# Kernel tuning notes

Hardware: AMD Instinct MI355X
Metric: run time of the kernel (lower is better)

Reference implementation:

```python
import jax, jax.numpy as jnp
import numpy as np

PATCH_SIZES = (16, 32, 48, 64)
RES_IDX = (0, 1, 2, 3)  # min(int(s*4/3), 3) for s in 0..3
QUANT_RESI = 0.5
BETA = 0.25
D = 32      # embedding_dim == input channels
V = 2048    # vocab_size
G = 8       # GroupNorm groups
EPS = 1e-5


def conv3(x, w, b):
    y = jax.lax.conv_general_dilated(x, w, (1, 1), 'SAME', dimension_numbers=('NCHW', 'OIHW', 'NCHW'))
    return y + b[None, :, None, None]


def group_norm(x, gamma, beta):
    n, c, h, w = x.shape
    xr = x.reshape(n, G, c // G, h, w)
    mu = xr.mean(axis=(2, 3, 4), keepdims=True)
    var = xr.var(axis=(2, 3, 4), keepdims=True)
    xn = ((xr - mu) * jax.lax.rsqrt(var + EPS)).reshape(n, c, h, w)
    return xn * gamma[None, :, None, None] + beta[None, :, None, None]


def conv_block(x, w1, b1, gamma, beta, w2, b2):
    h = conv3(x, w1, b1)
    h = jax.nn.gelu(group_norm(h, gamma, beta), approximate=False)
    return conv3(h, w2, b2)


def _forward(x, emb, pw1, pb1, pg, pbt, pw2, pb2, rw1, rb1, rg, rbt, rw2, rb2):
    B, C, H, W = x.shape
    acc = jnp.zeros_like(x)
    total_loss = jnp.zeros((), x.dtype)
    idx_list = []
    for s, p in enumerate(PATCH_SIZES):
        nh, nw = H // p, W // p
        # unfold: non-overlapping patches -> (B*N, C, p, p), N row-major over (nh, nw)
        patches = (x - acc).reshape(B, C, nh, p, nw, p).transpose(0, 2, 4, 1, 3, 5).reshape(B * nh * nw, C, p, p)
        z = conv_block(patches, pw1[s], pb1[s], pg[s], pbt[s], pw2[s], pb2[s])
        zf = z.reshape(-1, D)  # raw row-major reshape, exactly as the torch code does
        d = (zf * zf).sum(1, keepdims=True) + (emb * emb).sum(1) - 2.0 * (zf @ emb.T)
        idx = jnp.argmin(d, axis=1)
        zq = emb[idx].reshape(z.shape)
        loss = jnp.mean((jax.lax.stop_gradient(zq) - z) ** 2) + BETA * jnp.mean((zq - jax.lax.stop_gradient(z)) ** 2)
        total_loss = total_loss + loss
        zq = z + jax.lax.stop_gradient(zq - z)  # straight-through estimator
        r = RES_IDX[s]
        zq = zq * (1.0 - QUANT_RESI) + conv_block(zq, rw1[r], rb1[r], rg[r], rbt[r], rw2[r], rb2[r]) * QUANT_RESI
        # fold: exact inverse of unfold (patch sizes divide H, W)
        decoded = zq.reshape(B, nh, nw, C, p, p).transpose(0, 3, 1, 4, 2, 5).reshape(B, C, H, W)
        acc = acc + decoded
        idx_list.append(idx.reshape(B, -1))
    return (jax.nn.sigmoid(acc), *idx_list, total_loss)


def setup_inputs() -> dict:
    key = jax.random.key(0)
    ks = jax.random.split(key, 4)
    S = len(PATCH_SIZES)
    x = jax.random.normal(ks[0], (1, D, 384, 384), dtype=jnp.float32)
    emb = jax.random.uniform(ks[1], (V, D), jnp.float32, -1.0 / V, 1.0 / V)

    def wset(k):
        k1, k2, k3, k4 = jax.random.split(k, 4)
        return (jax.random.normal(k1, (S, D, D, 3, 3), jnp.float32) * 0.05,
                jax.random.normal(k2, (S, D), jnp.float32) * 0.02,
                jnp.ones((S, D), jnp.float32),
                jnp.zeros((S, D), jnp.float32),
                jax.random.normal(k3, (S, D, D, 3, 3), jnp.float32) * 0.05,
                jax.random.normal(k4, (S, D), jnp.float32) * 0.02)

    pw1, pb1, pg, pbt, pw2, pb2 = wset(ks[2])
    rw1, rb1, rg, rbt, rw2, rb2 = wset(ks[3])
    return {"x": x, "emb": emb,
            "pw1": pw1, "pb1": pb1, "pg": pg, "pbt": pbt, "pw2": pw2, "pb2": pb2,
            "rw1": rw1, "rb1": rb1, "rg": rg, "rbt": rbt, "rw2": rw2, "rb2": rb2}


def reference(x, emb, pw1, pb1, pg, pbt, pw2, pb2, rw1, rb1, rg, rbt, rw2, rb2):
    return _forward(x, emb, pw1, pb1, pg, pbt, pw2, pb2, rw1, rb1, rg, rbt, rw2, rb2)
```

## Files before the change

### kernel.cpp

```cpp
#include <hip/hip_runtime.h>
#include <cmath>

#define WIDTH 384
#define HW 147456
#define CHW 4718592
#define NCH 32
#define NV 2048
#define NROWS 147456

typedef short vshort8 __attribute__((ext_vector_type(8)));
typedef float vfloat4 __attribute__((ext_vector_type(4)));

__device__ inline unsigned short bf_split(float x, float& back) {
  unsigned int b; __builtin_memcpy(&b, &x, 4);
  unsigned int r = (b + 0x7FFFu + ((b >> 16) & 1u)) >> 16;
  unsigned int bb = r << 16; float f; __builtin_memcpy(&f, &bb, 4);
  back = f; return (unsigned short)r;
}

template <int SQ>
__device__ float np_pw(const float* a, int n, float mu) {
  if (n < 8) {
    float res = 0.0f;
    for (int i = 0; i < n; i++) {
      float v = a[i];
      if (SQ) { float d = __fsub_rn(v, mu); v = __fmul_rn(d, d); }
      res = __fadd_rn(res, v);
    }
    return res;
  }
  if (n <= 128) {
    float r[8];
#pragma unroll
    for (int j = 0; j < 8; j++) {
      float v = a[j];
      if (SQ) { float d = __fsub_rn(v, mu); v = __fmul_rn(d, d); }
      r[j] = v;
    }
    int i;
    for (i = 8; i + 8 <= n; i += 8) {
#pragma unroll
      for (int j = 0; j < 8; j++) {
        float v = a[i + j];
        if (SQ) { float d = __fsub_rn(v, mu); v = __fmul_rn(d, d); }
        r[j] = __fadd_rn(r[j], v);
      }
    }
    float res = __fadd_rn(__fadd_rn(__fadd_rn(r[0], r[1]), __fadd_rn(r[2], r[3])),
                          __fadd_rn(__fadd_rn(r[4], r[5]), __fadd_rn(r[6], r[7])));
    for (; i < n; i++) {
      float v = a[i];
      if (SQ) { float d = __fsub_rn(v, mu); v = __fmul_rn(d, d); }
      res = __fadd_rn(res, v);
    }
    return res;
  }
  int n2 = n / 2; n2 -= n2 % 8;
  return __fadd_rn(np_pw<SQ>(a, n2, mu), np_pw<SQ>(a + n2, n - n2, mu));
}

__global__ __launch_bounds__(256) void prep_kernel(
    const float* __restrict__ pw1, const float* __restrict__ pw2,
    const float* __restrict__ rw1, const float* __restrict__ rw2,
    const float* __restrict__ emb, float* __restrict__ wt, float* __restrict__ ee,
    unsigned short* __restrict__ eh, unsigned short* __restrict__ el) {
  int t = blockIdx.x * 256 + threadIdx.x;
  if (t < 147456) {
    int layer = t / 9216, r = t % 9216;
    int k = r / 32, co = r % 32;
    int set = layer >> 2, s = layer & 3;
    const float* src = set == 0 ? pw1 : set == 1 ? pw2 : set == 2 ? rw1 : rw2;
    wt[t] = src[s * 9216 + co * 288 + k];
  } else if (t < 147456 + NV) {
    int v = t - 147456;
    const float* e = emb + v * 32;
    float r[8];
#pragma unroll
    for (int j = 0; j < 8; j++) r[j] = __fmul_rn(e[j], e[j]);
#pragma unroll
    for (int i = 8; i < 32; i += 8)
#pragma unroll
      for (int j = 0; j < 8; j++) r[j] = __fadd_rn(r[j], __fmul_rn(e[i + j], e[i + j]));
    ee[v] = __fadd_rn(__fadd_rn(__fadd_rn(r[0], r[1]), __fadd_rn(r[2], r[3])),
                      __fadd_rn(__fadd_rn(r[4], r[5]), __fadd_rn(r[6], r[7])));
  } else if (t < 147456 + NV + 65536) {
    int idx = t - 147456 - NV;
    float x = emb[idx], hb;
    eh[idx] = bf_split(x, hb);
    float lb;
    el[idx] = bf_split(__fsub_rn(x, hb), lb);
  }
}

template <int MODE>
__global__ __launch_bounds__(192, 3) void conv32_kernel(
    const float* __restrict__ in, const float* __restrict__ x,
    const float* __restrict__ accin, float* __restrict__ outb,
    const float* __restrict__ zqb, float* __restrict__ acc,
    const float* __restrict__ wt, const float* __restrict__ bias, int p, int nw) {
  int t = blockIdx.x * 192 + threadIdx.x;
  int pp = p * p;
  int px = t % p; int t1 = t / p;
  int py = t1 % p;
  int n  = t1 / p;
  int i = n / nw, j = n % nw;

  int off[9]; bool msk[9];
#pragma unroll
  for (int dy = 0; dy < 3; dy++) {
    int ly = py + dy - 1;
    bool vy = (unsigned)ly < (unsigned)p;
    int cy = vy ? ly : 0;
#pragma unroll
    for (int dx = 0; dx < 3; dx++) {
      int lx = px + dx - 1;
      bool vx = (unsigned)lx < (unsigned)p;
      int cx = vx ? lx : 0;
      msk[dy * 3 + dx] = vy && vx;
      if (MODE == 1) off[dy * 3 + dx] = (i * p + cy) * WIDTH + (j * p + cx);
      else           off[dy * 3 + dx] = cy * p + cx;
    }
  }

  const float* pin = (MODE == 1) ? nullptr : in + (size_t)n * NCH * pp;

  float a[NCH];
#pragma unroll
  for (int co = 0; co < NCH; co++) a[co] = 0.0f;

  float tv[9], tn[9];
#pragma unroll
  for (int k = 0; k < 9; k++) {
    float v;
    if (MODE == 1) {
      size_t ad = (size_t)off[k];
      v = __fsub_rn(x[ad], accin[ad]);
    } else {
      v = pin[off[k]];
    }
    tv[k] = msk[k] ? v : 0.0f;
  }

  for (int ci = 0; ci < NCH; ci++) {
    if (ci + 1 < NCH) {
#pragma unroll
      for (int k = 0; k < 9; k++) {
        float v;
        if (MODE == 1) {
          size_t ad = (size_t)(ci + 1) * HW + off[k];
          v = __fsub_rn(x[ad], accin[ad]);
        } else {
          v = pin[(size_t)(ci + 1) * pp + off[k]];
        }
        tn[k] = msk[k] ? v : 0.0f;
      }
    }
    const float* wp = wt + ci * 288;
#pragma unroll
    for (int k = 0; k < 9; k++) {
#pragma unroll
      for (int co = 0; co < NCH; co++)
        a[co] = fmaf(tv[k], wp[k * 32 + co], a[co]);
    }
#pragma unroll
    for (int k = 0; k < 9; k++) tv[k] = tn[k];
  }

#pragma unroll
  for (int co = 0; co < NCH; co++) {
    float r = __fadd_rn(a[co], bias[co]);
    if (MODE == 2) {
      size_t img = (size_t)co * HW + (size_t)(i * p + py) * WIDTH + (j * p + px);
      size_t pt  = (size_t)n * NCH * pp + (size_t)co * pp + (size_t)py * p + px;
      float dec = __fadd_rn(__fmul_rn(zqb[pt], 0.5f), __fmul_rn(r, 0.5f));
      acc[img] = __fadd_rn(acc[img], dec);
    } else {
      outb[(size_t)n * NCH * pp + (size_t)co * pp + (size_t)py * p + px] = r;
    }
  }
}

__global__ __launch_bounds__(64) void gn_stats_kernel(
    const float* __restrict__ buf, float2* __restrict__ stats,
    int p, int C, int chunk) {
  int tid = threadIdx.x;
  int gpw = 64 / C;
  int gi = tid / C, cl = tid % C;
  int grp = blockIdx.x * gpw + gi;
  int pp = p * p, ne = 4 * pp;
  const float* base = buf + ((size_t)(grp >> 3) * NCH + (size_t)(grp & 7) * 4) * pp
                      + (size_t)cl * chunk;

  float s = np_pw<0>(base, chunk, 0.0f);
  for (int m = 1; m < C; m <<= 1) s = __fadd_rn(s, __shfl_xor(s, m, 64));
  float mu = __fdiv_rn(s, (float)ne);

  float s2 = np_pw<1>(base, chunk, mu);
  for (int m = 1; m < C; m <<= 1) s2 = __fadd_rn(s2, __shfl_xor(s2, m, 64));

  if (cl == 0) {
    float var = __fdiv_rn(s2, (float)ne);
    float rs = __fdiv_rn(1.0f, __fsqrt_rn(__fadd_rn(var, 1e-5f)));
    stats[grp] = make_float2(mu, rs);
  }
}

__global__ __launch_bounds__(256) void gn_gelu_kernel(
    float* __restrict__ buf, const float2* __restrict__ stats,
    const float* __restrict__ gamma, const float* __restrict__ beta, int p) {
  int t = blockIdx.x * 256 + threadIdx.x;
  int pp = p * p;
  int t2 = t / pp;
  int c = t2 % NCH;
  int n = t2 / NCH;
  float2 st = stats[n * 8 + (c >> 2)];
  float v = __fadd_rn(__fmul_rn(__fmul_rn(__fsub_rn(buf[t], st.x), st.y), gamma[c]), beta[c]);
  float tt = __fdiv_rn(v, 1.41421356237309504880f);
  float e = (float)erf((double)tt);
  buf[t] = __fmul_rn(__fmul_rn(0.5f, v), __fadd_rn(1.0f, e));
}

__global__ __launch_bounds__(192) void zsplit_kernel(
    const float* __restrict__ z, unsigned short* __restrict__ zh,
    unsigned short* __restrict__ zl, float* __restrict__ zz) {
  int r = blockIdx.x * 192 + threadIdx.x;
  const float* zr = z + (size_t)r * 32;
  float zv[32];
#pragma unroll
  for (int q = 0; q < 32; q++) zv[q] = zr[q];

  float rr[8];
#pragma unroll
  for (int j = 0; j < 8; j++) rr[j] = __fmul_rn(zv[j], zv[j]);
#pragma unroll
  for (int i = 8; i < 32; i += 8)
#pragma unroll
    for (int j = 0; j < 8; j++) rr[j] = __fadd_rn(rr[j], __fmul_rn(zv[i + j], zv[i + j]));
  zz[r] = __fadd_rn(__fadd_rn(__fadd_rn(rr[0], rr[1]), __fadd_rn(rr[2], rr[3])),
                    __fadd_rn(__fadd_rn(rr[4], rr[5]), __fadd_rn(rr[6], rr[7])));

  unsigned short hbits[32], lbits[32];
#pragma unroll
  for (int q = 0; q < 32; q++) {
    float hb;
    hbits[q] = bf_split(zv[q], hb);
    float lb;
    lbits[q] = bf_split(__fsub_rn(zv[q], hb), lb);
  }
#pragma unroll
  for (int c = 0; c < 4; c++) {
    vshort8 hv, lv;
#pragma unroll
    for (int j = 0; j < 8; j++) { hv[j] = (short)hbits[c * 8 + j]; lv[j] = (short)lbits[c * 8 + j]; }
    *(vshort8*)(zh + (size_t)r * 32 + c * 8) = hv;
    *(vshort8*)(zl + (size_t)r * 32 + c * 8) = lv;
  }
}

__global__ __launch_bounds__(576, 5) void gemm_min_kernel(
    const unsigned short* __restrict__ ZH, const unsigned short* __restrict__ ZL,
    const float* __restrict__ ZZ,
    const unsigned short* __restrict__ EH, const unsigned short* __restrict__ EL,
    const float* __restrict__ EE,
    float* __restrict__ BD, float* __restrict__ B2, int* __restrict__ I1) {
  __shared__ float ee_l[2048];
  int tid = threadIdx.x;
  for (int i = tid; i < 2048; i += 576) ee_l[i] = EE[i];
  __syncthreads();

  int wid = tid / 64, lane = tid & 63;
  int t0 = blockIdx.x * 18 + wid * 2;
  int lr = lane & 15, lg = lane >> 4;

  vshort8 azh0 = *(const vshort8*)(ZH + (size_t)(t0 * 16 + lr) * 32 + 8 * lg);
  vshort8 azl0 = *(const vshort8*)(ZL + (size_t)(t0 * 16 + lr) * 32 + 8 * lg);
  vshort8 azh1 = *(const vshort8*)(ZH + (size_t)((t0 + 1) * 16 + lr) * 32 + 8 * lg);
  vshort8 azl1 = *(const vshort8*)(ZL + (size_t)((t0 + 1) * 16 + lr) * 32 + 8 * lg);
  float zzv[8];
#pragma unroll
  for (int r = 0; r < 4; r++) {
    zzv[r]     = ZZ[t0 * 16 + 4 * lg + r];
    zzv[4 + r] = ZZ[(t0 + 1) * 16 + 4 * lg + r];
  }

  float b1[8], b2[8]; int i1[8];
#pragma unroll
  for (int r = 0; r < 8; r++) { b1[r] = 3.402823466e+38f; b2[r] = 3.402823466e+38f; i1[r] = 0; }

  vshort8 nbeh = *(const vshort8*)(EH + (size_t)lr * 32 + 8 * lg);
  vshort8 nbel = *(const vshort8*)(EL + (size_t)lr * 32 + 8 * lg);

  for (int ct = 0; ct < 128; ct++) {
    vshort8 beh = nbeh, bel = nbel;
    if (ct + 1 < 128) {
      nbeh = *(const vshort8*)(EH + (size_t)((ct + 1) * 16 + lr) * 32 + 8 * lg);
      nbel = *(const vshort8*)(EL + (size_t)((ct + 1) * 16 + lr) * 32 + 8 * lg);
    }
    vfloat4 acc0 = {0.0f, 0.0f, 0.0f, 0.0f};
    acc0 = __builtin_amdgcn_mfma_f32_16x16x32_bf16(azh0, beh, acc0, 0, 0, 0);
    acc0 = __builtin_amdgcn_mfma_f32_16x16x32_bf16(azh0, bel, acc0, 0, 0, 0);
    acc0 = __builtin_amdgcn_mfma_f32_16x16x32_bf16(azl0, beh, acc0, 0, 0, 0);
    vfloat4 acc1 = {0.0f, 0.0f, 0.0f, 0.0f};
    acc1 = __builtin_amdgcn_mfma_f32_16x16x32_bf16(azh1, beh, acc1, 0, 0, 0);
    acc1 = __builtin_amdgcn_mfma_f32_16x16x32_bf16(azh1, bel, acc1, 0, 0, 0);
    acc1 = __builtin_amdgcn_mfma_f32_16x16x32_bf16(azl1, beh, acc1, 0, 0, 0);
    int col = ct * 16 + lr;
    float eev = ee_l[col];
#pragma unroll
    for (int r = 0; r < 4; r++) {
      float d = (zzv[r] + eev) - 2.0f * acc0[r];
      if (d < b1[r]) { b2[r] = b1[r]; b1[r] = d; i1[r] = col; }
      else b2[r] = fminf(b2[r], d);
      float d1 = (zzv[4 + r] + eev) - 2.0f * acc1[r];
      if (d1 < b1[4 + r]) { b2[4 + r] = b1[4 + r]; b1[4 + r] = d1; i1[4 + r] = col; }
      else b2[4 + r] = fminf(b2[4 + r], d1);
    }
  }

  for (int m = 1; m < 16; m <<= 1) {
#pragma unroll
    for (int r = 0; r < 8; r++) {
      float ob1 = __shfl_xor(b1[r], m, 64);
      int   oi1 = __shfl_xor(i1[r], m, 64);
      float ob2 = __shfl_xor(b2[r], m, 64);
      bool aw = (b1[r] < ob1) || (b1[r] == ob1 && i1[r] < oi1);
      float lo = aw ? ob1 : b1[r];
      b1[r] = aw ? b1[r] : ob1;
      i1[r] = aw ? i1[r] : oi1;
      b2[r] = fminf(fminf(b2[r], ob2), lo);
    }
  }

  if (lr == 0) {
#pragma unroll
    for (int r = 0; r < 4; r++) {
      int row0 = t0 * 16 + 4 * lg + r;
      BD[row0] = b1[r]; B2[row0] = b2[r]; I1[row0] = i1[r];
      int row1 = (t0 + 1) * 16 + 4 * lg + r;
      BD[row1] = b1[4 + r]; B2[row1] = b2[4 + r]; I1[row1] = i1[4 + r];
    }
  }
}

__global__ __launch_bounds__(192) void finalize_kernel(
    const float* __restrict__ z, const float* __restrict__ emb,
    const float* __restrict__ EE, const float* __restrict__ ZZ,
    const float* __restrict__ BD, const float* __restrict__ B2,
    const int* __restrict__ I1, float* __restrict__ zq,
    float* __restrict__ idxout, double* __restrict__ part) {
  __shared__ double red[192];
  int tid = threadIdx.x;
  int lane = tid & 63;
  int r = blockIdx.x * 192 + tid;
  const float* zr = z + (size_t)r * 32;

  float zv[32];
#pragma unroll
  for (int q = 0; q < 32; q++) zv[q] = zr[q];

  float bd = BD[r];
  int bi = I1[r];
  float margin = __fadd_rn(1.0e-6f, __fmul_rn(5.0e-7f, fabsf(bd)));
  bool flagged = (B2[r] - bd) <= margin;

  unsigned long long mask = __ballot(flagged);
  while (mask) {
    int l = __ffsll((long long)mask) - 1;
    mask &= mask - 1;
    float zb[32];
#pragma unroll
    for (int q = 0; q < 32; q++) zb[q] = __shfl(zv[q], l, 64);
    int rl = __shfl(r, l, 64);
    float zzb = ZZ[rl];
    float bestd = 3.402823466e+38f;
    int bestv = NV;
    for (int k = 0; k < 32; k++) {
      int v = lane + 64 * k;
      const float* e0 = emb + (size_t)v * 32;
      float m = 0.0f;
#pragma unroll
      for (int q = 0; q < 32; q++) m = fmaf(zb[q], e0[q], m);
      float d = __fsub_rn(__fadd_rn(zzb, EE[v]), __fmul_rn(2.0f, m));
      if (d < bestd) { bestd = d; bestv = v; }
    }
    for (int mm = 1; mm < 64; mm <<= 1) {
      float od = __shfl_xor(bestd, mm, 64);
      int ov = __shfl_xor(bestv, mm, 64);
      if (od < bestd || (od == bestd && ov < bestv)) { bestd = od; bestv = ov; }
    }
    if (lane == l) bi = bestv;
  }

  double sse = 0.0;
  const float* ep = emb + (size_t)bi * 32;
#pragma unroll
  for (int q = 0; q < 32; q++) {
    float e = ep[q];
    zq[(size_t)r * 32 + q] = e;
    double dd = (double)e - (double)zv[q];
    sse += dd * dd;
  }
  idxout[r] = (float)bi;

  red[tid] = sse;
  __syncthreads();
  if (tid < 64) red[tid] = red[tid] + red[tid + 64] + red[tid + 128];
  __syncthreads();
  for (int st = 32; st > 0; st >>= 1) {
    if (tid < st) red[tid] += red[tid + st];
    __syncthreads();
  }
  if (tid == 0) part[blockIdx.x] = red[0];
}

__global__ __launch_bounds__(256) void sigmoid_kernel(
    const float* __restrict__ acc, float* __restrict__ out) {
  int t = blockIdx.x * 256 + threadIdx.x;
  out[t] = (float)(1.0 / (1.0 + exp(-(double)acc[t])));
}

__global__ void loss_kernel(const double* __restrict__ part, float* __restrict__ out) {
  double tot = 0.0;
  for (int s = 0; s < 4; s++) {
    double sse = 0.0;
    for (int b = 0; b < 768; b++) sse += part[s * 1024 + b];
    tot += 1.25 * sse / 4718592.0;
  }
  out[0] = (float)tot;
}

extern "C" void kernel_launch(void* const* d_in, const int* in_sizes, int n_in,
                              void* d_out, int out_size, void* d_ws, size_t ws_size,
                              hipStream_t stream) {
  const float* X   = (const float*)d_in[0];
  const float* EMB = (const float*)d_in[1];
  const float* PW1 = (const float*)d_in[2];
  const float* PB1 = (const float*)d_in[3];
  const float* PG  = (const float*)d_in[4];
  const float* PBT = (const float*)d_in[5];
  const float* PW2 = (const float*)d_in[6];
  const float* PB2 = (const float*)d_in[7];
  const float* RW1 = (const float*)d_in[8];
  const float* RB1 = (const float*)d_in[9];
  const float* RG  = (const float*)d_in[10];
  const float* RBT = (const float*)d_in[11];
  const float* RW2 = (const float*)d_in[12];
  const float* RB2 = (const float*)d_in[13];
  float* out = (float*)d_out;

  char* w = (char*)d_ws;
  float*          EE    = (float*)(w);
  float*          WT    = (float*)(w + 8192UL);
  unsigned short* EH    = (unsigned short*)(w + 598016UL);
  unsigned short* EL    = (unsigned short*)(w + 729088UL);
  float2*         STATS = (float2*)(w + 860160UL);
  double*         PART  = (double*)(w + 897024UL);
  float*          ZZ    = (float*)(w + 929792UL);
  float*          BD    = (float*)(w + 1519616UL);
  float*          B2    = (float*)(w + 2109440UL);
  int*            I1    = (int*)(w + 2699264UL);
  unsigned short* ZH    = (unsigned short*)(w + 3289088UL);
  unsigned short* ZL    = (unsigned short*)(w + 12726272UL);
  float*          P     = (float*)(w + 22163456UL);
  float*          H     = (float*)(w + 41037824UL);
  float*          ACC   = (float*)(w + 59912192UL);

  hipMemsetAsync(ACC, 0, 18874368UL, stream);
  prep_kernel<<<840, 256, 0, stream>>>(PW1, PW2, RW1, RW2, EMB, WT, EE, EH, EL);

  const int PS[4] = {16, 32, 48, 64};
  for (int s = 0; s < 4; s++) {
    int p = PS[s], nw = 384 / p, N = nw * nw;
    int C = (p == 16) ? 8 : (p == 32) ? 32 : 64;
    int chunk = (4 * p * p) / C;
    int gblocks = (N * 8 * C) / 64;
    const float* wt_p1 = WT + (0 * 4 + s) * 9216;
    const float* wt_p2 = WT + (1 * 4 + s) * 9216;
    const float* wt_r1 = WT + (2 * 4 + s) * 9216;
    const float* wt_r2 = WT + (3 * 4 + s) * 9216;

    conv32_kernel<1><<<768, 192, 0, stream>>>(nullptr, X, ACC, H, nullptr, nullptr,
                                              wt_p1, PB1 + s * 32, p, nw);
    gn_stats_kernel<<<gblocks, 64, 0, stream>>>(H, STATS, p, C, chunk);
    gn_gelu_kernel<<<18432, 256, 0, stream>>>(H, STATS, PG + s * 32, PBT + s * 32, p);
    conv32_kernel<0><<<768, 192, 0, stream>>>(H, nullptr, nullptr, P, nullptr, nullptr,
                                              wt_p2, PB2 + s * 32, p, nw);
    zsplit_kernel<<<768, 192, 0, stream>>>(P, ZH, ZL, ZZ);
    gemm_min_kernel<<<512, 576, 0, stream>>>(ZH, ZL, ZZ, EH, EL, EE, BD, B2, I1);
    finalize_kernel<<<768, 192, 0, stream>>>(P, EMB, EE, ZZ, BD, B2, I1, H,
                                             out + 4718592 + s * 147456, PART + s * 1024);
    conv32_kernel<0><<<768, 192, 0, stream>>>(H, nullptr, nullptr, P, nullptr, nullptr,
                                              wt_r1, RB1 + s * 32, p, nw);
    gn_stats_kernel<<<gblocks, 64, 0, stream>>>(P, STATS, p, C, chunk);
    gn_gelu_kernel<<<18432, 256, 0, stream>>>(P, STATS, RG + s * 32, RBT + s * 32, p);
    conv32_kernel<2><<<768, 192, 0, stream>>>(P, nullptr, nullptr, nullptr, H, ACC,
                                              wt_r2, RB2 + s * 32, p, nw);
  }

  sigmoid_kernel<<<18432, 256, 0, stream>>>(ACC, out);
  loss_kernel<<<1, 1, 0, stream>>>(PART, out + 5308416);
}
```

Baseline: 2.205 ms.

## Fuse VQ finalize step into the GEMM argmin kernel

Merges finalize_kernel into gemm_min_kernel: best/second-best distances and indices stay in shared memory instead of going through global BD/B2/I1 buffers. Near-tie rows get an exact fp32 recheck by one wave per row, which now reads z from global and EE from shared memory. Then the block writes zq and idx and reduces the SSE partials. This removes a kernel launch and the global round trip, but adds shared memory use and serialized per-wave recheck work inside the GEMM kernel, which may lower occupancy.

```diff
diff --git a/kernel.cpp b/kernel.cpp
--- a/kernel.cpp
+++ b/kernel.cpp
@@ -261,9 +261,13 @@
     const unsigned short* __restrict__ ZH, const unsigned short* __restrict__ ZL,
     const float* __restrict__ ZZ,
     const unsigned short* __restrict__ EH, const unsigned short* __restrict__ EL,
-    const float* __restrict__ EE,
-    float* __restrict__ BD, float* __restrict__ B2, int* __restrict__ I1) {
+    const float* __restrict__ EE, const float* __restrict__ z,
+    const float* __restrict__ emb, float* __restrict__ zq,
+    float* __restrict__ idxout, double* __restrict__ part) {
   __shared__ float ee_l[2048];
+  __shared__ int bi_l[288];
+  __shared__ int fl_l[288];
+  __shared__ double red[576];
   int tid = threadIdx.x;
   for (int i = tid; i < 2048; i += 576) ee_l[i] = EE[i];
   __syncthreads();
@@ -334,53 +338,36 @@
   if (lr == 0) {
 #pragma unroll
     for (int r = 0; r < 4; r++) {
-      int row0 = t0 * 16 + 4 * lg + r;
-      BD[row0] = b1[r]; B2[row0] = b2[r]; I1[row0] = i1[r];
-      int row1 = (t0 + 1) * 16 + 4 * lg + r;
-      BD[row1] = b1[4 + r]; B2[row1] = b2[4 + r]; I1[row1] = i1[4 + r];
-    }
-  }
-}
-
-__global__ __launch_bounds__(192) void finalize_kernel(
-    const float* __restrict__ z, const float* __restrict__ emb,
-    const float* __restrict__ EE, const float* __restrict__ ZZ,
-    const float* __restrict__ BD, const float* __restrict__ B2,
-    const int* __restrict__ I1, float* __restrict__ zq,
-    float* __restrict__ idxout, double* __restrict__ part) {
-  __shared__ double red[192];
-  int tid = threadIdx.x;
-  int lane = tid & 63;
-  int r = blockIdx.x * 192 + tid;
-  const float* zr = z + (size_t)r * 32;
-
-  float zv[32];
-#pragma unroll
-  for (int q = 0; q < 32; q++) zv[q] = zr[q];
-
-  float bd = BD[r];
-  int bi = I1[r];
-  float margin = __fadd_rn(1.0e-6f, __fmul_rn(5.0e-7f, fabsf(bd)));
-  bool flagged = (B2[r] - bd) <= margin;
-
-  unsigned long long mask = __ballot(flagged);
-  while (mask) {
-    int l = __ffsll((long long)mask) - 1;
-    mask &= mask - 1;
+      int l0 = wid * 32 + 4 * lg + r;
+      float mg0 = __fadd_rn(1.0e-6f, __fmul_rn(5.0e-7f, fabsf(b1[r])));
+      bi_l[l0] = i1[r];
+      fl_l[l0] = (b2[r] - b1[r]) <= mg0;
+      int l1 = wid * 32 + 16 + 4 * lg + r;
+      float mg1 = __fadd_rn(1.0e-6f, __fmul_rn(5.0e-7f, fabsf(b1[4 + r])));
+      bi_l[l1] = i1[4 + r];
+      fl_l[l1] = (b2[4 + r] - b1[4 + r]) <= mg1;
+    }
+  }
+  __syncthreads();
+
+  for (int k = 0; k < 32; k++) {
+    int lrow = wid * 32 + k;
+    if (!fl_l[lrow]) continue;
+    int rg = blockIdx.x * 288 + lrow;
+    const float* zp = z + (size_t)rg * 32;
     float zb[32];
 #pragma unroll
-    for (int q = 0; q < 32; q++) zb[q] = __shfl(zv[q], l, 64);
-    int rl = __shfl(r, l, 64);
-    float zzb = ZZ[rl];
+    for (int q = 0; q < 32; q++) zb[q] = zp[q];
+    float zzb = ZZ[rg];
     float bestd = 3.402823466e+38f;
     int bestv = NV;
-    for (int k = 0; k < 32; k++) {
-      int v = lane + 64 * k;
+    for (int kk = 0; kk < 32; kk++) {
+      int v = lane + 64 * kk;
       const float* e0 = emb + (size_t)v * 32;
       float m = 0.0f;
 #pragma unroll
       for (int q = 0; q < 32; q++) m = fmaf(zb[q], e0[q], m);
-      float d = __fsub_rn(__fadd_rn(zzb, EE[v]), __fmul_rn(2.0f, m));
+      float d = __fsub_rn(__fadd_rn(zzb, ee_l[v]), __fmul_rn(2.0f, m));
       if (d < bestd) { bestd = d; bestv = v; }
     }
     for (int mm = 1; mm < 64; mm <<= 1) {
@@ -388,23 +375,32 @@
       int ov = __shfl_xor(bestv, mm, 64);
       if (od < bestd || (od == bestd && ov < bestv)) { bestd = od; bestv = ov; }
     }
-    if (lane == l) bi = bestv;
-  }
-
+    if (lane == 0) bi_l[lrow] = bestv;
+  }
+  __syncthreads();
+
+  int lrow = tid >> 1, half = tid & 1;
+  int rg = blockIdx.x * 288 + lrow;
+  int bi = bi_l[lrow];
+  const float* ep = emb + (size_t)bi * 32 + half * 16;
+  const float* zr = z + (size_t)rg * 32 + half * 16;
   double sse = 0.0;
-  const float* ep = emb + (size_t)bi * 32;
-#pragma unroll
-  for (int q = 0; q < 32; q++) {
+#pragma unroll
+  for (int q = 0; q < 16; q++) {
     float e = ep[q];
-    zq[(size_t)r * 32 + q] = e;
-    double dd = (double)e - (double)zv[q];
+    zq[(size_t)rg * 32 + half * 16 + q] = e;
+    double dd = (double)e - (double)zr[q];
     sse += dd * dd;
   }
-  idxout[r] = (float)bi;
+  if (half == 0) idxout[rg] = (float)bi;
 
   red[tid] = sse;
   __syncthreads();
-  if (tid < 64) red[tid] = red[tid] + red[tid + 64] + red[tid + 128];
+  if (tid < 64) {
+    double s = red[tid];
+    for (int j = tid + 64; j < 576; j += 64) s += red[j];
+    red[tid] = s;
+  }
   __syncthreads();
   for (int st = 32; st > 0; st >>= 1) {
     if (tid < st) red[tid] += red[tid + st];
@@ -423,7 +419,7 @@
   double tot = 0.0;
   for (int s = 0; s < 4; s++) {
     double sse = 0.0;
-    for (int b = 0; b < 768; b++) sse += part[s * 1024 + b];
+    for (int b = 0; b < 512; b++) sse += part[s * 1024 + b];
     tot += 1.25 * sse / 4718592.0;
   }
   out[0] = (float)tot;
@@ -456,9 +452,6 @@
   float2*         STATS = (float2*)(w + 860160UL);
   double*         PART  = (double*)(w + 897024UL);
   float*          ZZ    = (float*)(w + 929792UL);
-  float*          BD    = (float*)(w + 1519616UL);
-  float*          B2    = (float*)(w + 2109440UL);
-  int*            I1    = (int*)(w + 2699264UL);
   unsigned short* ZH    = (unsigned short*)(w + 3289088UL);
   unsigned short* ZL    = (unsigned short*)(w + 12726272UL);
   float*          P     = (float*)(w + 22163456UL);
@@ -486,8 +479,7 @@
     conv32_kernel<0><<<768, 192, 0, stream>>>(H, nullptr, nullptr, P, nullptr, nullptr,
                                               wt_p2, PB2 + s * 32, p, nw);
     zsplit_kernel<<<768, 192, 0, stream>>>(P, ZH, ZL, ZZ);
-    gemm_min_kernel<<<512, 576, 0, stream>>>(ZH, ZL, ZZ, EH, EL, EE, BD, B2, I1);
-    finalize_kernel<<<768, 192, 0, stream>>>(P, EMB, EE, ZZ, BD, B2, I1, H,
+    gemm_min_kernel<<<512, 576, 0, stream>>>(ZH, ZL, ZZ, EH, EL, EE, P, EMB, H,
                                              out + 4718592 + s * 147456, PART + s * 1024);
     conv32_kernel<0><<<768, 192, 0, stream>>>(H, nullptr, nullptr, P, nullptr, nullptr,
                                               wt_r1, RB1 + s * 32, p, nw);
```

Measured after the change: 2.347 ms. +6.4%, slower.

## Split finalize into epilogue, compacted rescore list, and separate SSE reduction

Applied to the files above, without the earlier changes.

Replaces the per-row finalize kernel with three kernels. A vectorized epilogue writes zq, idx and per-quarter-row SSE partials and atomically appends near-tie rows to a list. A rescore kernel then recomputes exact distances only for the listed rows, one wavefront per row, and a separate kernel reduces the SSE partials. This removes the wave-serialized ballot loop that stalled whole waves whenever one row was flagged. It adds two kernel launches, an atomic counter and extra global traffic for the partials.

```diff
diff --git a/kernel.cpp b/kernel.cpp
--- a/kernel.cpp
+++ b/kernel.cpp
@@ -342,36 +342,56 @@
   }
 }
 
-__global__ __launch_bounds__(192) void finalize_kernel(
+__global__ __launch_bounds__(256) void epilogue_kernel(
+    const float* __restrict__ z, const float* __restrict__ emb,
+    const float* __restrict__ BD, const float* __restrict__ B2,
+    const int* __restrict__ I1, float* __restrict__ zq,
+    float* __restrict__ idxout, double* __restrict__ ssep,
+    int* __restrict__ list, int* __restrict__ cnt) {
+  int t = blockIdx.x * 256 + threadIdx.x;
+  int row = t >> 2, part = t & 3;
+  float bd = BD[row];
+  int bi = I1[row];
+  float margin = __fadd_rn(1.0e-6f, __fmul_rn(5.0e-7f, fabsf(bd)));
+  bool flagged = (B2[row] - bd) <= margin;
+  if (flagged && part == 0) {
+    int i = atomicAdd(cnt, 1);
+    list[i] = row;
+  }
+  const float4* ep = (const float4*)(emb + (size_t)bi * 32 + part * 8);
+  const float4* zp = (const float4*)(z + (size_t)row * 32 + part * 8);
+  float4* qp = (float4*)(zq + (size_t)row * 32 + part * 8);
+  float4 e0 = ep[0], e1 = ep[1];
+  float4 z0 = zp[0], z1 = zp[1];
+  qp[0] = e0; qp[1] = e1;
+  double sse = 0.0, d;
+  d = (double)e0.x - (double)z0.x; sse += d * d;
+  d = (double)e0.y - (double)z0.y; sse += d * d;
+  d = (double)e0.z - (double)z0.z; sse += d * d;
+  d = (double)e0.w - (double)z0.w; sse += d * d;
+  d = (double)e1.x - (double)z1.x; sse += d * d;
+  d = (double)e1.y - (double)z1.y; sse += d * d;
+  d = (double)e1.z - (double)z1.z; sse += d * d;
+  d = (double)e1.w - (double)z1.w; sse += d * d;
+  ssep[t] = sse;
+  if (part == 0) idxout[row] = (float)bi;
+}
+
+__global__ __launch_bounds__(64) void rescore_kernel(
     const float* __restrict__ z, const float* __restrict__ emb,
     const float* __restrict__ EE, const float* __restrict__ ZZ,
-    const float* __restrict__ BD, const float* __restrict__ B2,
-    const int* __restrict__ I1, float* __restrict__ zq,
-    float* __restrict__ idxout, double* __restrict__ part) {
-  __shared__ double red[192];
-  int tid = threadIdx.x;
-  int lane = tid & 63;
-  int r = blockIdx.x * 192 + tid;
-  const float* zr = z + (size_t)r * 32;
-
-  float zv[32];
-#pragma unroll
-  for (int q = 0; q < 32; q++) zv[q] = zr[q];
-
-  float bd = BD[r];
-  int bi = I1[r];
-  float margin = __fadd_rn(1.0e-6f, __fmul_rn(5.0e-7f, fabsf(bd)));
-  bool flagged = (B2[r] - bd) <= margin;
-
-  unsigned long long mask = __ballot(flagged);
-  while (mask) {
-    int l = __ffsll((long long)mask) - 1;
-    mask &= mask - 1;
+    float* __restrict__ zq, float* __restrict__ idxout,
+    double* __restrict__ ssep, const int* __restrict__ list,
+    const int* __restrict__ cnt) {
+  int lane = threadIdx.x;
+  int n = *cnt;
+  for (int i = blockIdx.x; i < n; i += gridDim.x) {
+    int row = list[i];
+    const float* zp = z + (size_t)row * 32;
     float zb[32];
 #pragma unroll
-    for (int q = 0; q < 32; q++) zb[q] = __shfl(zv[q], l, 64);
-    int rl = __shfl(r, l, 64);
-    float zzb = ZZ[rl];
+    for (int q = 0; q < 32; q++) zb[q] = zp[q];
+    float zzb = ZZ[row];
     float bestd = 3.402823466e+38f;
     int bestv = NV;
     for (int k = 0; k < 32; k++) {
@@ -388,29 +408,34 @@
       int ov = __shfl_xor(bestv, mm, 64);
       if (od < bestd || (od == bestd && ov < bestv)) { bestd = od; bestv = ov; }
     }
-    if (lane == l) bi = bestv;
-  }
-
-  double sse = 0.0;
-  const float* ep = emb + (size_t)bi * 32;
-#pragma unroll
-  for (int q = 0; q < 32; q++) {
-    float e = ep[q];
-    zq[(size_t)r * 32 + q] = e;
-    double dd = (double)e - (double)zv[q];
-    sse += dd * dd;
-  }
-  idxout[r] = (float)bi;
-
-  red[tid] = sse;
+    if (lane < 32) zq[(size_t)row * 32 + lane] = emb[bestv * 32 + lane];
+    if (lane < 4) {
+      const float* ep = emb + bestv * 32 + lane * 8;
+      const float* zr = z + (size_t)row * 32 + lane * 8;
+      double sse = 0.0;
+#pragma unroll
+      for (int q = 0; q < 8; q++) {
+        double dd = (double)ep[q] - (double)zr[q];
+        sse += dd * dd;
+      }
+      ssep[row * 4 + lane] = sse;
+    }
+    if (lane == 0) idxout[row] = (float)bestv;
+  }
+}
+
+__global__ __launch_bounds__(256) void ssered_kernel(
+    const double* __restrict__ ssep, double* __restrict__ part) {
+  __shared__ double red[256];
+  int t = blockIdx.x * 256 + threadIdx.x;
+  const double* b = ssep + (size_t)t * 4;
+  red[threadIdx.x] = ((b[0] + b[1]) + (b[2] + b[3]));
   __syncthreads();
-  if (tid < 64) red[tid] = red[tid] + red[tid + 64] + red[tid + 128];
-  __syncthreads();
-  for (int st = 32; st > 0; st >>= 1) {
-    if (tid < st) red[tid] += red[tid + st];
+  for (int st = 128; st > 0; st >>= 1) {
+    if (threadIdx.x < st) red[threadIdx.x] += red[threadIdx.x + st];
     __syncthreads();
   }
-  if (tid == 0) part[blockIdx.x] = red[0];
+  if (threadIdx.x == 0) part[blockIdx.x] = red[0];
 }
 
 __global__ __launch_bounds__(256) void sigmoid_kernel(
@@ -423,7 +448,7 @@
   double tot = 0.0;
   for (int s = 0; s < 4; s++) {
     double sse = 0.0;
-    for (int b = 0; b < 768; b++) sse += part[s * 1024 + b];
+    for (int b = 0; b < 576; b++) sse += part[s * 1024 + b];
     tot += 1.25 * sse / 4718592.0;
   }
   out[0] = (float)tot;
@@ -464,8 +489,12 @@
   float*          P     = (float*)(w + 22163456UL);
   float*          H     = (float*)(w + 41037824UL);
   float*          ACC   = (float*)(w + 59912192UL);
+  int*            CNT   = (int*)(w + 78786560UL);
+  int*            LIST  = (int*)(w + 78786624UL);
+  double*         SSEP  = (double*)(w + 79376448UL);
 
   hipMemsetAsync(ACC, 0, 18874368UL, stream);
+  hipMemsetAsync(CNT, 0, 64UL, stream);
   prep_kernel<<<840, 256, 0, stream>>>(PW1, PW2, RW1, RW2, EMB, WT, EE, EH, EL);
 
   const int PS[4] = {16, 32, 48, 64};
@@ -487,8 +516,13 @@
                                               wt_p2, PB2 + s * 32, p, nw);
     zsplit_kernel<<<768, 192, 0, stream>>>(P, ZH, ZL, ZZ);
     gemm_min_kernel<<<512, 576, 0, stream>>>(ZH, ZL, ZZ, EH, EL, EE, BD, B2, I1);
-    finalize_kernel<<<768, 192, 0, stream>>>(P, EMB, EE, ZZ, BD, B2, I1, H,
-                                             out + 4718592 + s * 147456, PART + s * 1024);
+    epilogue_kernel<<<2304, 256, 0, stream>>>(P, EMB, BD, B2, I1, H,
+                                              out + 4718592 + s * 147456, SSEP,
+                                              LIST, CNT + s);
+    rescore_kernel<<<1024, 64, 0, stream>>>(P, EMB, EE, ZZ, H,
+                                            out + 4718592 + s * 147456, SSEP,
+                                            LIST, CNT + s);
+    ssered_kernel<<<576, 256, 0, stream>>>(SSEP, PART + s * 1024);
     conv32_kernel<0><<<768, 192, 0, stream>>>(H, nullptr, nullptr, P, nullptr, nullptr,
                                               wt_r1, RB1 + s * 32, p, nw);
     gn_stats_kernel<<<gblocks, 64, 0, stream>>>(P, STATS, p, C, chunk);
```

Result: faster. 2.071 ms (-6.1%).
